# Kernel optimization log

Measured on AMD Instinct MI355X. Metric: run time of the kernel, lower is better.

## Reference

```python
import jax, jax.numpy as jnp
import numpy as np


def setup_inputs() -> dict:
    key = jax.random.key(0)
    k1, k2 = jax.random.split(key)
    B, S, D = 16, 4096, 512
    xs = jax.random.normal(k1, (B, S, D), dtype=jnp.float32)
    # lengths in [1, S] so the mean is always well-defined (torch would NaN on 0)
    xs_len = jax.random.randint(k2, (B,), 1, S + 1, dtype=jnp.int64)
    return {"xs": xs, "xs_len": xs_len}


def reference(xs, xs_len):
    # Masked mean over the first xs_len[b] positions of each sequence.
    # Equivalent to torch.stack([x[:l].mean(dim=-2) for x, l in zip(xs, xs_len)])
    B, S, D = xs.shape
    mask = (jnp.arange(S)[None, :] < xs_len[:, None])  # [B, S]
    summed = jnp.einsum('bsd,bs->bd', xs, mask.astype(xs.dtype))  # [B, D]
    return summed / xs_len.astype(xs.dtype)[:, None]
```

## Files before the change

kernel.cpp:

```cpp
#include <hip/hip_runtime.h>
#include <hip/hip_bf16.h>


#define THREADS 128
#define CHUNKS  64

__global__ __launch_bounds__(THREADS) void mean_embed_kernel(
    const float* __restrict__ xs,
    const int*   __restrict__ xs_len,
    float*       __restrict__ out,
    int S, int D)
{
    const int b     = blockIdx.x;
    const int chunk = blockIdx.y;
    const int L     = xs_len[b];

    const int rows_per_blk = S / CHUNKS;
    const int row0 = chunk * rows_per_blk;
    if (row0 >= L) return;
    const int row1 = min(row0 + rows_per_blk, L);

    const int tid = threadIdx.x;
    const int d4  = D >> 2;

    const float4* base = (const float4*)(xs + (size_t)b * S * D);

    float4 acc = make_float4(0.f, 0.f, 0.f, 0.f);
    for (int s = row0; s < row1; ++s) {
        float4 v = base[(size_t)s * d4 + tid];
        acc.x += v.x; acc.y += v.y; acc.z += v.z; acc.w += v.w;
    }

    const float inv = 1.0f / (float)L;
    float* o = out + (size_t)b * D + tid * 4;
    atomicAdd(o + 0, acc.x * inv);
    atomicAdd(o + 1, acc.y * inv);
    atomicAdd(o + 2, acc.z * inv);
    atomicAdd(o + 3, acc.w * inv);
}

extern "C" void kernel_launch(void* const* d_in, const int* in_sizes, int n_in,
                              void* d_out, int out_size, void* d_ws, size_t ws_size,
                              hipStream_t stream) {
    const float* xs     = (const float*)d_in[0];
    const int*   xs_len = (const int*)d_in[1];
    float*       out    = (float*)d_out;

    const int B = in_sizes[1];
    const int total = in_sizes[0];
    const int D = 512;
    const int S = total / (B * D);

    hipMemsetAsync(d_out, 0, (size_t)out_size * sizeof(float), stream);

    dim3 grid(B, CHUNKS);
    mean_embed_kernel<<<grid, THREADS, 0, stream>>>(xs, xs_len, out, S, D);
}
```

Measured before the change: 199.7 us.

## Split masked mean into finer-grained partial sums plus second-stage reduction

Replaces the atomic-based single kernel with a two-stage reduction. Stage one uses many small 16-row chunks with an unrolled load loop and writes per-chunk partial sums to workspace. Stage two reduces valid chunks per batch and scales by the length. The aim is more parallelism and memory-level concurrency without the memset and atomics, at the cost of an extra launch and workspace traffic.

New measurement: 191.8 us. 4.0% less time.

```diff
diff --git a/kernel.cpp b/kernel.cpp
--- a/kernel.cpp
+++ b/kernel.cpp
@@ -1,58 +1,98 @@
 #include <hip/hip_runtime.h>
-#include <hip/hip_bf16.h>
 
 
-#define THREADS 128
-#define CHUNKS  64
+#define ROWS   16
+#define T1     128
+#define T2     128
 
-__global__ __launch_bounds__(THREADS) void mean_embed_kernel(
-    const float* __restrict__ xs,
-    const int*   __restrict__ xs_len,
-    float*       __restrict__ out,
-    int S, int D)
+__global__ __launch_bounds__(T1) void mean_embed_stage1(
+    const float4* __restrict__ xs,
+    const int*    __restrict__ xs_len,
+    float4*       __restrict__ ws,
+    int S, int nchunks)
 {
     const int b     = blockIdx.x;
     const int chunk = blockIdx.y;
     const int L     = xs_len[b];
+    const int row0  = chunk * ROWS;
+    if (row0 >= L) return;
+    const int row1 = min(row0 + ROWS, L);
+    const int tid  = threadIdx.x;
 
-    const int rows_per_blk = S / CHUNKS;
-    const int row0 = chunk * rows_per_blk;
-    if (row0 >= L) return;
-    const int row1 = min(row0 + rows_per_blk, L);
-
-    const int tid = threadIdx.x;
-    const int d4  = D >> 2;
-
-    const float4* base = (const float4*)(xs + (size_t)b * S * D);
+    const float4* base = xs + (size_t)b * S * T1;
 
     float4 acc = make_float4(0.f, 0.f, 0.f, 0.f);
-    for (int s = row0; s < row1; ++s) {
-        float4 v = base[(size_t)s * d4 + tid];
+    if (row1 - row0 == ROWS) {
+        #pragma unroll
+        for (int i = 0; i < ROWS; ++i) {
+            float4 v = base[(size_t)(row0 + i) * T1 + tid];
+            acc.x += v.x; acc.y += v.y; acc.z += v.z; acc.w += v.w;
+        }
+    } else {
+        for (int s = row0; s < row1; ++s) {
+            float4 v = base[(size_t)s * T1 + tid];
+            acc.x += v.x; acc.y += v.y; acc.z += v.z; acc.w += v.w;
+        }
+    }
+
+    ws[((size_t)b * nchunks + chunk) * T1 + tid] = acc;
+}
+
+__global__ __launch_bounds__(T2) void mean_embed_stage2(
+    const float4* __restrict__ ws,
+    const int*    __restrict__ xs_len,
+    float4*       __restrict__ out,
+    int nchunks)
+{
+    const int b   = blockIdx.x;
+    const int tid = threadIdx.x;
+    const int col = blockIdx.y * 32 + (tid & 31);
+    const int cl  = tid >> 5;
+    const int L   = xs_len[b];
+    const int nch = (L + ROWS - 1) / ROWS;
+
+    float4 acc = make_float4(0.f, 0.f, 0.f, 0.f);
+    for (int c = cl; c < nch; c += 4) {
+        float4 v = ws[((size_t)b * nchunks + c) * T1 + col];
         acc.x += v.x; acc.y += v.y; acc.z += v.z; acc.w += v.w;
     }
 
-    const float inv = 1.0f / (float)L;
-    float* o = out + (size_t)b * D + tid * 4;
-    atomicAdd(o + 0, acc.x * inv);
-    atomicAdd(o + 1, acc.y * inv);
-    atomicAdd(o + 2, acc.z * inv);
-    atomicAdd(o + 3, acc.w * inv);
+    __shared__ float4 red[T2];
+    red[tid] = acc;
+    __syncthreads();
+
+    if (tid < 32) {
+        float4 a0 = red[tid];
+        float4 a1 = red[tid + 32];
+        float4 a2 = red[tid + 64];
+        float4 a3 = red[tid + 96];
+        const float inv = 1.0f / (float)L;
+        float4 r;
+        r.x = (a0.x + a1.x + a2.x + a3.x) * inv;
+        r.y = (a0.y + a1.y + a2.y + a3.y) * inv;
+        r.z = (a0.z + a1.z + a2.z + a3.z) * inv;
+        r.w = (a0.w + a1.w + a2.w + a3.w) * inv;
+        out[(size_t)b * T1 + col] = r;
+    }
 }
 
 extern "C" void kernel_launch(void* const* d_in, const int* in_sizes, int n_in,
                               void* d_out, int out_size, void* d_ws, size_t ws_size,
                               hipStream_t stream) {
-    const float* xs     = (const float*)d_in[0];
-    const int*   xs_len = (const int*)d_in[1];
-    float*       out    = (float*)d_out;
+    const float4* xs     = (const float4*)d_in[0];
+    const int*    xs_len = (const int*)d_in[1];
+    float4*       out    = (float4*)d_out;
+    float4*       ws     = (float4*)d_ws;
 
     const int B = in_sizes[1];
     const int total = in_sizes[0];
     const int D = 512;
     const int S = total / (B * D);
+    const int nchunks = (S + ROWS - 1) / ROWS;
 
-    hipMemsetAsync(d_out, 0, (size_t)out_size * sizeof(float), stream);
+    dim3 g1(B, nchunks);
+    mean_embed_stage1<<<g1, T1, 0, stream>>>(xs, xs_len, ws, S, nchunks);
 
-    dim3 grid(B, CHUNKS);
-    mean_embed_kernel<<<grid, THREADS, 0, stream>>>(xs, xs_len, out, S, D);
+    dim3 g2(B, 4);
+    mean_embed_stage2<<<g2, T2, 0, stream>>>(ws, xs_len, out, nchunks);
 }
```

## Replace float atomics with per-chunk partials and last-block reduction

Applied to the files above, without the earlier changes.

Blocks grow to 512 threads, with four row-subgroups summing a 64-row slab that is then reduced in shared memory. Each block writes its partial sum to workspace, and the last block per batch, found through an atomic counter, does the final reduction and scale. This removes the float atomicAdds and the memset of the output and raises parallelism per block. In exchange it adds workspace traffic and threadfence synchronisation, and the result now depends on the workspace being large enough.

Measured after the change: 235.1 us. 17.8% more time.

```diff
diff --git a/kernel.cpp b/kernel.cpp
--- a/kernel.cpp
+++ b/kernel.cpp
@@ -1,58 +1,103 @@
 #include <hip/hip_runtime.h>
-#include <hip/hip_bf16.h>
 
 
-#define THREADS 128
-#define CHUNKS  64
+#define T      512
+#define D4     128
+#define SLAB   64
+#define SUB    16
+#define NCHMAX 64
 
-__global__ __launch_bounds__(THREADS) void mean_embed_kernel(
-    const float* __restrict__ xs,
-    const int*   __restrict__ xs_len,
-    float*       __restrict__ out,
-    int S, int D)
+__device__ __forceinline__ float4 f4add(float4 a, float4 b) {
+    return make_float4(a.x + b.x, a.y + b.y, a.z + b.z, a.w + b.w);
+}
+
+__global__ __launch_bounds__(T) void mean_embed_fused(
+    const float4* __restrict__ xs,
+    const int*    __restrict__ xs_len,
+    float4*       __restrict__ part,
+    int*          __restrict__ cnt,
+    float4*       __restrict__ out,
+    int S)
 {
     const int b     = blockIdx.x;
     const int chunk = blockIdx.y;
     const int L     = xs_len[b];
-
-    const int rows_per_blk = S / CHUNKS;
-    const int row0 = chunk * rows_per_blk;
+    const int row0  = chunk * SLAB;
     if (row0 >= L) return;
-    const int row1 = min(row0 + rows_per_blk, L);
+    const int nch = (L + SLAB - 1) / SLAB;
 
     const int tid = threadIdx.x;
-    const int d4  = D >> 2;
+    const int col = tid & (D4 - 1);
+    const int sub = tid >> 7;
 
-    const float4* base = (const float4*)(xs + (size_t)b * S * D);
+    const float4* base = xs + (size_t)b * S * D4;
 
     float4 acc = make_float4(0.f, 0.f, 0.f, 0.f);
-    for (int s = row0; s < row1; ++s) {
-        float4 v = base[(size_t)s * d4 + tid];
-        acc.x += v.x; acc.y += v.y; acc.z += v.z; acc.w += v.w;
+    const int r0 = row0 + sub * SUB;
+    if (row0 + SLAB <= L) {
+        #pragma unroll
+        for (int i = 0; i < SUB; ++i)
+            acc = f4add(acc, base[(size_t)(r0 + i) * D4 + col]);
+    } else {
+        const int r1 = min(r0 + SUB, L);
+        for (int s = r0; s < r1; ++s)
+            acc = f4add(acc, base[(size_t)s * D4 + col]);
     }
 
-    const float inv = 1.0f / (float)L;
-    float* o = out + (size_t)b * D + tid * 4;
-    atomicAdd(o + 0, acc.x * inv);
-    atomicAdd(o + 1, acc.y * inv);
-    atomicAdd(o + 2, acc.z * inv);
-    atomicAdd(o + 3, acc.w * inv);
+    __shared__ float4 red[T];
+    red[tid] = acc;
+    __syncthreads();
+    if (tid < D4) {
+        float4 p = f4add(f4add(red[tid],        red[tid + 128]),
+                         f4add(red[tid + 256],  red[tid + 384]));
+        part[((size_t)b * NCHMAX + chunk) * D4 + tid] = p;
+    }
+    __syncthreads();
+
+    __shared__ int is_last;
+    if (tid == 0) {
+        __threadfence();
+        int old = atomicAdd(&cnt[b], 1);
+        is_last = (old == nch - 1);
+    }
+    __syncthreads();
+    if (!is_last) return;
+
+    __threadfence();
+
+    const int cl = tid >> 7;
+    float4 acc2 = make_float4(0.f, 0.f, 0.f, 0.f);
+    for (int c = cl; c < nch; c += 4)
+        acc2 = f4add(acc2, part[((size_t)b * NCHMAX + c) * D4 + col]);
+
+    red[tid] = acc2;
+    __syncthreads();
+    if (tid < D4) {
+        float4 s4 = f4add(f4add(red[tid],       red[tid + 128]),
+                          f4add(red[tid + 256], red[tid + 384]));
+        const float inv = 1.0f / (float)L;
+        out[(size_t)b * D4 + tid] =
+            make_float4(s4.x * inv, s4.y * inv, s4.z * inv, s4.w * inv);
+    }
 }
 
 extern "C" void kernel_launch(void* const* d_in, const int* in_sizes, int n_in,
                               void* d_out, int out_size, void* d_ws, size_t ws_size,
                               hipStream_t stream) {
-    const float* xs     = (const float*)d_in[0];
-    const int*   xs_len = (const int*)d_in[1];
-    float*       out    = (float*)d_out;
+    const float4* xs     = (const float4*)d_in[0];
+    const int*    xs_len = (const int*)d_in[1];
+    float4*       out    = (float4*)d_out;
 
     const int B = in_sizes[1];
     const int total = in_sizes[0];
     const int D = 512;
     const int S = total / (B * D);
 
-    hipMemsetAsync(d_out, 0, (size_t)out_size * sizeof(float), stream);
+    float4* part = (float4*)d_ws;
+    int*    cnt  = (int*)((char*)d_ws + (size_t)B * NCHMAX * D4 * sizeof(float4));
 
-    dim3 grid(B, CHUNKS);
-    mean_embed_kernel<<<grid, THREADS, 0, stream>>>(xs, xs_len, out, S, D);
+    hipMemsetAsync(cnt, 0, B * sizeof(int), stream);
+
+    dim3 grid(B, S / SLAB);
+    mean_embed_fused<<<grid, T, 0, stream>>>(xs, xs_len, part, cnt, out, S);
 }
```
